# Kernel tuning notes

Hardware: AMD Instinct MI355X
Metric: run time of the kernel (lower is better)

## Reference

```python
import jax, jax.numpy as jnp
import numpy as np

DT = 0.05
TAU = 0.15
SIGMA = float(np.sqrt(2.0 * DT / TAU))  # GaussianNoise default sigma
NOISE_SCALE = 1.0

N = 2048        # nneurons
RANK = 64       # nbg
BATCH = 2048
IN_DIM = 128    # input_sources['stim'] size


def setup_inputs() -> dict:
    key = jax.random.key(0)
    ks = jax.random.split(key, 10)
    inv_sqrt_n = 1.0 / np.sqrt(N)
    return {
        "r_thalamic": jax.random.uniform(ks[0], (BATCH, RANK), jnp.float32),
        "stim": jax.random.normal(ks[1], (BATCH, IN_DIM), jnp.float32),
        "x": jax.random.normal(ks[2], (BATCH, N), jnp.float32) * inv_sqrt_n,
        "r": jax.nn.softplus(jax.random.normal(ks[3], (BATCH, N), jnp.float32) * inv_sqrt_n),
        "J": jax.random.normal(ks[4], (N, N), jnp.float32) * (1.2 * inv_sqrt_n),
        "B": jax.random.normal(ks[5], (1, N), jnp.float32),
        "U": jax.random.normal(ks[6], (N, RANK), jnp.float32) * inv_sqrt_n,
        "V": jax.random.normal(ks[7], (RANK, N), jnp.float32) * inv_sqrt_n,
        "I_stim": jax.random.normal(ks[8], (IN_DIM, N), jnp.float32) * inv_sqrt_n,
        "eps": jax.random.normal(ks[9], (BATCH, N), jnp.float32),
    }


def reference(r_thalamic, stim, x, r, J, B, U, V, I_stim, eps):
    # external input: stim @ I['stim']  -> (batch, N)
    ext = stim @ I_stim
    # bg_tensor @ r == U @ diag(r_thalamic) @ V @ r, computed in low-rank form:
    # (batch, rank) * (batch, rank) -> project back with U
    rec_input = (r_thalamic * (r @ V.T)) @ U.T          # (batch, N)
    pre = -x + r @ J + rec_input + B + ext               # (batch, N)
    noisy = pre + (SIGMA * NOISE_SCALE) * eps            # GaussianNoise
    x_new = x + (DT / TAU) * noisy
    r_new = jax.nn.softplus(x_new)
    return (x_new, r_new)
```

## Files before the change

### kernel.cpp

```cpp
#include <hip/hip_runtime.h>
#include <cstdint>
#include <cstddef>


#define KA 2176
#define KB 2240
#define NN 2048

using frag_ab = __attribute__((ext_vector_type(8))) short;
using frag_cd = __attribute__((ext_vector_type(4))) float;

__device__ __forceinline__ unsigned short f2bf(float f) {
  union { float f; unsigned int i; } v;
  v.f = f;
  unsigned int r = v.i + 0x7fffu + ((v.i >> 16) & 1u);
  return (unsigned short)(r >> 16);
}

__device__ __forceinline__ uint4 cvt8(const float* __restrict__ p) {
  float4 a = *(const float4*)p;
  float4 b = *(const float4*)(p + 4);
  union { uint4 v; unsigned short u[8]; } d;
  d.u[0] = f2bf(a.x); d.u[1] = f2bf(a.y); d.u[2] = f2bf(a.z); d.u[3] = f2bf(a.w);
  d.u[4] = f2bf(b.x); d.u[5] = f2bf(b.y); d.u[6] = f2bf(b.z); d.u[7] = f2bf(b.w);
  return d.v;
}

__device__ __forceinline__ void gl_lds16(const void* g, void* l) {
  __builtin_amdgcn_global_load_lds(
      (const __attribute__((address_space(1))) void*)g,
      (__attribute__((address_space(3))) void*)l, 16, 0, 0);
}

__global__ __launch_bounds__(256) void prep(
    const float* __restrict__ J, const float* __restrict__ Ist,
    const float* __restrict__ rg, const float* __restrict__ stim,
    const float* __restrict__ U, const float* __restrict__ V,
    unsigned short* __restrict__ Ap, unsigned short* __restrict__ Bp,
    float* __restrict__ part) {
  __shared__ unsigned short tile[64 * 66];
  __shared__ alignas(16) unsigned short Ats[32 * 64];
  __shared__ alignas(16) unsigned short Bts[64 * 64];
  const int blk = blockIdx.x;
  const int t = threadIdx.x;

  if (blk < 1088) {
    const float* src;
    int dst_off, cx, cy;
    if (blk < 1024) { src = J;   dst_off = 0;    cx = blk & 31; cy = blk >> 5; }
    else            { src = Ist; dst_off = 2048; cx = (blk - 1024) & 31; cy = (blk - 1024) >> 5; }
    const int r0 = cy * 64, c0 = cx * 64;
    const int sr = t >> 3, c8 = t & 7;
#pragma unroll
    for (int p = 0; p < 2; ++p) {
      const int row = sr + 32 * p;
      union { uint4 v; unsigned short u[8]; } d;
      d.v = cvt8(&src[(size_t)(r0 + row) * 2048 + c0 + c8 * 8]);
#pragma unroll
      for (int e = 0; e < 8; ++e) tile[row * 66 + c8 * 8 + e] = d.u[e];
    }
    __syncthreads();
#pragma unroll
    for (int p = 0; p < 2; ++p) {
      const int scol = sr + 32 * p;
      union { uint4 v; unsigned short u[8]; } d;
#pragma unroll
      for (int e = 0; e < 8; ++e) d.u[e] = tile[(c8 * 8 + e) * 66 + scol];
      *(uint4*)&Bp[(size_t)(c0 + scol) * KB + dst_off + r0 + c8 * 8] = d.v;
    }
  } else if (blk < 3136) {
    const int row = blk - 1088;
    *(uint4*)&Ap[(size_t)row * KA + t * 8] = cvt8(&rg[(size_t)row * 2048 + t * 8]);
    if (t < 24) {
      const int c = 256 + t;
      if (c < 272)
        *(uint4*)&Ap[(size_t)row * KA + c * 8] =
            cvt8(&stim[(size_t)row * 128 + (c - 256) * 8]);
      else
        *(uint4*)&Bp[(size_t)row * KB + c * 8] =
            cvt8(&U[(size_t)row * 64 + (c - 272) * 8]);
    }
  } else {
    const int tb = blk - 3136;
    const int mt = tb & 63, s = tb >> 6;
    const int b0 = mt * 32;
    const int wave = t >> 6, lane = t & 63;
    const int q = lane >> 4, l15 = lane & 15;
    const int arow = t >> 3, ac8 = t & 7;

    const float* gA  = rg + (size_t)(b0 + arow) * 2048 + s * 512 + ac8 * 8;
    const float* gB0 = V  + (size_t)arow        * 2048 + s * 512 + ac8 * 8;
    const float* gB1 = V  + (size_t)(arow + 32) * 2048 + s * 512 + ac8 * 8;

    frag_cd acc0 = {0.f, 0.f, 0.f, 0.f};
    frag_cd acc1 = {0.f, 0.f, 0.f, 0.f};

    for (int kt = 0; kt < 8; ++kt) {
      const int k0 = kt * 64;
      uint4 va  = cvt8(gA + k0);
      uint4 vb0 = cvt8(gB0 + k0);
      uint4 vb1 = cvt8(gB1 + k0);
      __syncthreads();
      *(uint4*)&Ats[t * 8]        = va;
      *(uint4*)&Bts[t * 8]        = vb0;
      *(uint4*)&Bts[2048 + t * 8] = vb1;
      __syncthreads();
#pragma unroll
      for (int ks = 0; ks < 2; ++ks) {
        frag_ab a0 = *(const frag_ab*)&Ats[(l15)      * 64 + ks * 32 + q * 8];
        frag_ab a1 = *(const frag_ab*)&Ats[(16 + l15) * 64 + ks * 32 + q * 8];
        frag_ab b  = *(const frag_ab*)&Bts[(wave * 16 + l15) * 64 + ks * 32 + q * 8];
        acc0 = __builtin_amdgcn_mfma_f32_16x16x32_bf16(a0, b, acc0, 0, 0, 0);
        acc1 = __builtin_amdgcn_mfma_f32_16x16x32_bf16(a1, b, acc1, 0, 0, 0);
      }
    }
    const int p = wave * 16 + l15;
#pragma unroll
    for (int reg = 0; reg < 4; ++reg) {
      const int m0 = q * 4 + reg;
      part[((size_t)s * 2048 + b0 + m0) * 64 + p]      = acc0[reg];
      part[((size_t)s * 2048 + b0 + m0 + 16) * 64 + p] = acc1[reg];
    }
  }
}

__global__ __launch_bounds__(256, 4) void main_gemm(
    const unsigned short* __restrict__ Ap, const unsigned short* __restrict__ Bp,
    const float* __restrict__ part, const float* __restrict__ tha,
    const float* __restrict__ xg, const float* __restrict__ epsg,
    const float* __restrict__ Bvec,
    float* __restrict__ outx, float* __restrict__ outr) {
  __shared__ alignas(16) unsigned short As[64 * 64];
  __shared__ alignas(16) unsigned short Bs[64 * 64];

  const int t = threadIdx.x;
  const int wave = t >> 6, lane = t & 63;
  const int q = lane >> 4, l15 = lane & 15, l7 = lane & 7;
  const int wm = (wave & 1) * 32, wn = (wave >> 1) * 32;
  const int bm0 = blockIdx.y * 64, bn0 = blockIdx.x * 64;

  const unsigned short* gA[2];
  const unsigned short* gB[2];
  unsigned short* lA[2];
  unsigned short* lB[2];
  uint4 tval[2];
#pragma unroll
  for (int r = 0; r < 2; ++r) {
    const int ci = r * 256 + t;
    const int row = ci >> 3;
    const int lc = (ci & 7) ^ (row & 7);
    gA[r] = Ap + (size_t)(bm0 + row) * KA + lc * 8;
    gB[r] = Bp + (size_t)(bn0 + row) * KB + lc * 8;
    lA[r] = As + (size_t)(r * 256 + wave * 64) * 8;
    lB[r] = Bs + (size_t)(r * 256 + wave * 64) * 8;

    const int p0 = lc * 8;
    const size_t base = ((size_t)(bm0 + row)) * 64 + p0;
    float4 s0 = *(const float4*)&part[base];
    float4 s1 = *(const float4*)&part[base + 4];
#pragma unroll
    for (int s = 1; s < 4; ++s) {
      float4 a = *(const float4*)&part[(size_t)s * 131072 + base];
      float4 b = *(const float4*)&part[(size_t)s * 131072 + base + 4];
      s0.x += a.x; s0.y += a.y; s0.z += a.z; s0.w += a.w;
      s1.x += b.x; s1.y += b.y; s1.z += b.z; s1.w += b.w;
    }
    float4 th0 = *(const float4*)&tha[base];
    float4 th1 = *(const float4*)&tha[base + 4];
    union { uint4 v; unsigned short u[8]; } d;
    d.u[0] = f2bf(th0.x * s0.x); d.u[1] = f2bf(th0.y * s0.y);
    d.u[2] = f2bf(th0.z * s0.z); d.u[3] = f2bf(th0.w * s0.w);
    d.u[4] = f2bf(th1.x * s1.x); d.u[5] = f2bf(th1.y * s1.y);
    d.u[6] = f2bf(th1.z * s1.z); d.u[7] = f2bf(th1.w * s1.w);
    tval[r] = d.v;
  }

  frag_cd acc[2][2];
#pragma unroll
  for (int i = 0; i < 2; ++i)
#pragma unroll
    for (int j = 0; j < 2; ++j) {
      frag_cd z = {0.f, 0.f, 0.f, 0.f};
      acc[i][j] = z;
    }

#pragma unroll 1
  for (int kt = 0; kt < 34; ++kt) {
    const int k0 = kt * 64;
    __syncthreads();
#pragma unroll
    for (int r = 0; r < 2; ++r) {
      gl_lds16(gA[r] + k0, lA[r]);
      gl_lds16(gB[r] + k0, lB[r]);
    }
    __syncthreads();
#pragma unroll
    for (int ks = 0; ks < 2; ++ks) {
      const int lc = ks * 4 + q;
      frag_ab af[2], bfr[2];
#pragma unroll
      for (int i = 0; i < 2; ++i) {
        af[i]  = *(const frag_ab*)&As[(wm + i * 16 + l15) * 64 + ((lc ^ l7) * 8)];
        bfr[i] = *(const frag_ab*)&Bs[(wn + i * 16 + l15) * 64 + ((lc ^ l7) * 8)];
      }
#pragma unroll
      for (int i = 0; i < 2; ++i)
#pragma unroll
        for (int j = 0; j < 2; ++j)
          acc[i][j] = __builtin_amdgcn_mfma_f32_16x16x32_bf16(af[i], bfr[j], acc[i][j], 0, 0, 0);
    }
  }

  {
    const int k0 = 34 * 64;
    __syncthreads();
#pragma unroll
    for (int r = 0; r < 2; ++r) {
      *(uint4*)&As[(size_t)(r * 256 + t) * 8] = tval[r];
      gl_lds16(gB[r] + k0, lB[r]);
    }
    __syncthreads();
#pragma unroll
    for (int ks = 0; ks < 2; ++ks) {
      const int lc = ks * 4 + q;
      frag_ab af[2], bfr[2];
#pragma unroll
      for (int i = 0; i < 2; ++i) {
        af[i]  = *(const frag_ab*)&As[(wm + i * 16 + l15) * 64 + ((lc ^ l7) * 8)];
        bfr[i] = *(const frag_ab*)&Bs[(wn + i * 16 + l15) * 64 + ((lc ^ l7) * 8)];
      }
#pragma unroll
      for (int i = 0; i < 2; ++i)
#pragma unroll
        for (int j = 0; j < 2; ++j)
          acc[i][j] = __builtin_amdgcn_mfma_f32_16x16x32_bf16(af[i], bfr[j], acc[i][j], 0, 0, 0);
    }
  }

  const float A_DT = 0.33333334f;
  const float SIG  = 0.81649658092772615f;
#pragma unroll
  for (int j = 0; j < 2; ++j) {
    const int nc = bn0 + wn + j * 16 + l15;
    const float bvf = Bvec[nc];
#pragma unroll
    for (int i = 0; i < 2; ++i) {
#pragma unroll
      for (int reg = 0; reg < 4; ++reg) {
        const int mr = bm0 + wm + i * 16 + q * 4 + reg;
        const size_t off = (size_t)mr * NN + nc;
        const float xf = xg[off];
        const float ef = epsg[off];
        const float xn = xf + A_DT * (acc[i][j][reg] + bvf - xf + SIG * ef);
        outx[off] = xn;
        outr[off] = (xn > 20.f) ? xn : log1pf(__expf(xn));
      }
    }
  }
}

extern "C" void kernel_launch(void* const* d_in, const int* in_sizes, int n_in,
                              void* d_out, int out_size, void* d_ws, size_t ws_size,
                              hipStream_t stream) {
  (void)in_sizes; (void)n_in; (void)out_size; (void)ws_size;
  const float* tha  = (const float*)d_in[0];
  const float* stim = (const float*)d_in[1];
  const float* x    = (const float*)d_in[2];
  const float* r    = (const float*)d_in[3];
  const float* J    = (const float*)d_in[4];
  const float* Bv   = (const float*)d_in[5];
  const float* U    = (const float*)d_in[6];
  const float* V    = (const float*)d_in[7];
  const float* Ist  = (const float*)d_in[8];
  const float* eps  = (const float*)d_in[9];

  unsigned short* Apk = (unsigned short*)d_ws;
  unsigned short* Bpk = Apk + (size_t)NN * KA;
  float* part = (float*)(Bpk + (size_t)NN * KB);
  float* outx = (float*)d_out;
  float* outr = outx + (size_t)NN * NN;

  prep<<<3392, 256, 0, stream>>>(J, Ist, r, stim, U, V, Apk, Bpk, part);
  main_gemm<<<dim3(32, 32), 256, 0, stream>>>(Apk, Bpk, part, tha, x, eps, Bv,
                                              outx, outr);
}
```

Before: 181.1 us.

## Double-buffer main GEMM tiles via register prefetch instead of direct-to-LDS loads

Replaces the single-buffered global_load_lds loop, which used two barriers per K-tile, with a two-stage LDS ping-pong. Each next tile is prefetched into registers while the current one is computed. This cuts the loop to one barrier per tile and hides global load latency behind MFMA work. In exchange it doubles LDS use to 32KB per block, which may reduce occupancy under launch_bounds(256,4), and it routes loads through VGPRs, raising register pressure.

```diff
diff --git a/kernel.cpp b/kernel.cpp
--- a/kernel.cpp
+++ b/kernel.cpp
@@ -24,12 +24,6 @@
   d.u[0] = f2bf(a.x); d.u[1] = f2bf(a.y); d.u[2] = f2bf(a.z); d.u[3] = f2bf(a.w);
   d.u[4] = f2bf(b.x); d.u[5] = f2bf(b.y); d.u[6] = f2bf(b.z); d.u[7] = f2bf(b.w);
   return d.v;
-}
-
-__device__ __forceinline__ void gl_lds16(const void* g, void* l) {
-  __builtin_amdgcn_global_load_lds(
-      (const __attribute__((address_space(1))) void*)g,
-      (__attribute__((address_space(3))) void*)l, 16, 0, 0);
 }
 
 __global__ __launch_bounds__(256) void prep(
@@ -130,8 +124,8 @@
     const float* __restrict__ xg, const float* __restrict__ epsg,
     const float* __restrict__ Bvec,
     float* __restrict__ outx, float* __restrict__ outr) {
-  __shared__ alignas(16) unsigned short As[64 * 64];
-  __shared__ alignas(16) unsigned short Bs[64 * 64];
+  __shared__ alignas(16) unsigned short As[2 * 4096];
+  __shared__ alignas(16) unsigned short Bs[2 * 4096];
 
   const int t = threadIdx.x;
   const int wave = t >> 6, lane = t & 63;
@@ -141,21 +135,26 @@
 
   const unsigned short* gA[2];
   const unsigned short* gB[2];
-  unsigned short* lA[2];
-  unsigned short* lB[2];
-  uint4 tval[2];
+  const unsigned short* gBp[2];
+  int slot[2];
 #pragma unroll
   for (int r = 0; r < 2; ++r) {
     const int ci = r * 256 + t;
     const int row = ci >> 3;
     const int lc = (ci & 7) ^ (row & 7);
-    gA[r] = Ap + (size_t)(bm0 + row) * KA + lc * 8;
-    gB[r] = Bp + (size_t)(bn0 + row) * KB + lc * 8;
-    lA[r] = As + (size_t)(r * 256 + wave * 64) * 8;
-    lB[r] = Bs + (size_t)(r * 256 + wave * 64) * 8;
-
-    const int p0 = lc * 8;
-    const size_t base = ((size_t)(bm0 + row)) * 64 + p0;
+    gA[r]  = Ap + (size_t)(bm0 + row) * KA + lc * 8;
+    gB[r]  = Bp + (size_t)(bn0 + row) * KB + lc * 8;
+    gBp[r] = Bp + (size_t)(bn0 + row) * KB + 2176 + lc * 8;
+    slot[r] = ci * 8;
+  }
+
+  uint4 tval[2];
+#pragma unroll
+  for (int r = 0; r < 2; ++r) {
+    const int ci = r * 256 + t;
+    const int row = ci >> 3;
+    const int lc = (ci & 7) ^ (row & 7);
+    const size_t base = ((size_t)(bm0 + row)) * 64 + lc * 8;
     float4 s0 = *(const float4*)&part[base];
     float4 s1 = *(const float4*)&part[base + 4];
 #pragma unroll
@@ -184,24 +183,15 @@
       acc[i][j] = z;
     }
 
-#pragma unroll 1
-  for (int kt = 0; kt < 34; ++kt) {
-    const int k0 = kt * 64;
-    __syncthreads();
-#pragma unroll
-    for (int r = 0; r < 2; ++r) {
-      gl_lds16(gA[r] + k0, lA[r]);
-      gl_lds16(gB[r] + k0, lB[r]);
-    }
-    __syncthreads();
+  auto compute_tile = [&](int abase) {
 #pragma unroll
     for (int ks = 0; ks < 2; ++ks) {
       const int lc = ks * 4 + q;
       frag_ab af[2], bfr[2];
 #pragma unroll
       for (int i = 0; i < 2; ++i) {
-        af[i]  = *(const frag_ab*)&As[(wm + i * 16 + l15) * 64 + ((lc ^ l7) * 8)];
-        bfr[i] = *(const frag_ab*)&Bs[(wn + i * 16 + l15) * 64 + ((lc ^ l7) * 8)];
+        af[i]  = *(const frag_ab*)&As[abase + (wm + i * 16 + l15) * 64 + ((lc ^ l7) * 8)];
+        bfr[i] = *(const frag_ab*)&Bs[abase + (wn + i * 16 + l15) * 64 + ((lc ^ l7) * 8)];
       }
 #pragma unroll
       for (int i = 0; i < 2; ++i)
@@ -209,32 +199,62 @@
         for (int j = 0; j < 2; ++j)
           acc[i][j] = __builtin_amdgcn_mfma_f32_16x16x32_bf16(af[i], bfr[j], acc[i][j], 0, 0, 0);
     }
+  };
+
+  uint4 cA[2], cB[2], nA[2], nB[2];
+#pragma unroll
+  for (int r = 0; r < 2; ++r) {
+    cA[r] = *(const uint4*)gA[r];
+    cB[r] = *(const uint4*)gB[r];
+  }
+
+#pragma unroll 1
+  for (int p = 0; p < 17; ++p) {
+    {
+      const int k1 = (2 * p + 1) * 64;
+#pragma unroll
+      for (int r = 0; r < 2; ++r) {
+        nA[r] = *(const uint4*)(gA[r] + k1);
+        nB[r] = *(const uint4*)(gB[r] + k1);
+      }
+#pragma unroll
+      for (int r = 0; r < 2; ++r) {
+        *(uint4*)&As[slot[r]] = cA[r];
+        *(uint4*)&Bs[slot[r]] = cB[r];
+      }
+      __syncthreads();
+      compute_tile(0);
+    }
+    {
+      if (p < 16) {
+        const int k2 = (2 * p + 2) * 64;
+#pragma unroll
+        for (int r = 0; r < 2; ++r) {
+          cA[r] = *(const uint4*)(gA[r] + k2);
+          cB[r] = *(const uint4*)(gB[r] + k2);
+        }
+      } else {
+#pragma unroll
+        for (int r = 0; r < 2; ++r) cB[r] = *(const uint4*)gBp[r];
+      }
+#pragma unroll
+      for (int r = 0; r < 2; ++r) {
+        *(uint4*)&As[4096 + slot[r]] = nA[r];
+        *(uint4*)&Bs[4096 + slot[r]] = nB[r];
+      }
+      __syncthreads();
+      compute_tile(4096);
+    }
   }
 
   {
-    const int k0 = 34 * 64;
+#pragma unroll
+    for (int r = 0; r < 2; ++r) {
+      *(uint4*)&As[slot[r]] = tval[r];
+      *(uint4*)&Bs[slot[r]] = cB[r];
+    }
     __syncthreads();
-#pragma unroll
-    for (int r = 0; r < 2; ++r) {
-      *(uint4*)&As[(size_t)(r * 256 + t) * 8] = tval[r];
-      gl_lds16(gB[r] + k0, lB[r]);
-    }
-    __syncthreads();
-#pragma unroll
-    for (int ks = 0; ks < 2; ++ks) {
-      const int lc = ks * 4 + q;
-      frag_ab af[2], bfr[2];
-#pragma unroll
-      for (int i = 0; i < 2; ++i) {
-        af[i]  = *(const frag_ab*)&As[(wm + i * 16 + l15) * 64 + ((lc ^ l7) * 8)];
-        bfr[i] = *(const frag_ab*)&Bs[(wn + i * 16 + l15) * 64 + ((lc ^ l7) * 8)];
-      }
-#pragma unroll
-      for (int i = 0; i < 2; ++i)
-#pragma unroll
-        for (int j = 0; j < 2; ++j)
-          acc[i][j] = __builtin_amdgcn_mfma_f32_16x16x32_bf16(af[i], bfr[j], acc[i][j], 0, 0, 0);
-    }
+    compute_tile(0);
   }
 
   const float A_DT = 0.33333334f;
```

After: 348.8 us. 1.93x slower.
